# Kernel optimization log

Measured on AMD Instinct MI355X. Metric: run time of the kernel, lower is better.

Reference implementation:

```python
import jax, jax.numpy as jnp
import numpy as np

D = 256   # model dim
M = 64    # num mechanisms
B = 4
S = 8192


def setup_inputs() -> dict:
    key = jax.random.key(0)
    ks = jax.random.split(key, 16)
    n = jax.random.normal
    inp = {
        "x": n(ks[0], (B, S, D), jnp.float32),
        "context": n(ks[1], (B, S, D), jnp.float32),
        # stacked per-mechanism params (m, out, in) etc.
        "Wm": n(ks[2], (M, D, D), jnp.float32) * (1.0 / np.sqrt(D)),
        "bm": n(ks[3], (M, D), jnp.float32) * 0.02,
        "cm": n(ks[4], (M, D), jnp.float32),           # characteristics (1,1,dim) per node
        "um": n(ks[5], (M, D), jnp.float32) * (1.0 / np.sqrt(D)),  # timing_gate weight
        "vm": n(ks[6], (M,), jnp.float32) * 0.02,       # timing_gate bias
        # selector: Linear(d, 2d) -> GELU -> Linear(2d, m)
        "W1": n(ks[7], (2 * D, D), jnp.float32) * (1.0 / np.sqrt(D)),
        "b1": n(ks[8], (2 * D,), jnp.float32) * 0.02,
        "W2": n(ks[9], (M, 2 * D), jnp.float32) * (1.0 / np.sqrt(2 * D)),
        "b2": n(ks[10], (M,), jnp.float32) * 0.02,
        # integrate: Linear(2d, d)
        "Wi": n(ks[11], (D, 2 * D), jnp.float32) * (1.0 / np.sqrt(2 * D)),
        "bi": n(ks[12], (D,), jnp.float32) * 0.02,
    }
    return inp


def reference(x, context, Wm, bm, cm, um, vm, W1, b1, W2, b2, Wi, bi):
    # selector: softmax over mechanisms (b, s, m)
    h = jax.nn.gelu(jnp.einsum('bsd,ed->bse', context, W1) + b1, approximate=False)
    scores = jax.nn.softmax(jnp.einsum('bse,me->bsm', h, W2) + b2, axis=-1)

    # per-mechanism sigmoid timing gate (b, s, m)
    gate = jax.nn.sigmoid(jnp.einsum('bsd,md->bsm', x, um) + vm)

    # combined weight a[b,s,m] = softmax_score * gate; then
    # selected = sum_m a * (x @ Wm.T + bm + cm)  -- contracted without
    # materializing the (b, s, m, d) stack the torch loop builds.
    a = scores * gate                               # (b, s, m)
    selected = jnp.einsum('bsm,bse,mde->bsd', a, x, Wm) \
             + jnp.einsum('bsm,md->bsd', a, bm + cm)

    # integrate(concat([x, selected]))
    cat = jnp.concatenate([x, selected], axis=-1)   # (b, s, 2d)
    integrated = jnp.einsum('bse,de->bsd', cat, Wi) + bi
    return integrated
```

## Files before the change

### kernel.cpp

```cpp
#include <hip/hip_runtime.h>
#include <cstdint>
#include <cstddef>


typedef _Float16 f16;
typedef f16 f16x8 __attribute__((ext_vector_type(8)));
typedef float f32x4 __attribute__((ext_vector_type(4)));
typedef float f32x16 __attribute__((ext_vector_type(16)));

#define DEV __device__ __forceinline__

DEV uint32_t swz128(uint32_t b) { return b ^ (((b >> 7) & 7u) << 4); }

DEV void gload_lds16(const void* g, void* l) {
  __builtin_amdgcn_global_load_lds(
      (const __attribute__((address_space(1))) unsigned int*)g,
      (__attribute__((address_space(3))) unsigned int*)l, 16, 0, 0);
}

DEV f16x8 cvt8(float4 u0, float4 u1) {
  f16x8 v = {(f16)u0.x, (f16)u0.y, (f16)u0.z, (f16)u0.w,
             (f16)u1.x, (f16)u1.y, (f16)u1.z, (f16)u1.w};
  return v;
}

__global__ void prep_b_kernel(const float* __restrict__ S, f16* __restrict__ dst,
                              int K, int BN, int total) {
  int t = blockIdx.x * 256 + threadIdx.x;
  if (t >= total) return;
  int gpc = BN * 8;
  int g = t % gpc;
  int c = (t / gpc) % (K / 64);
  int cb = t / (gpc * (K / 64));
  int ks = g / (BN * 4);
  int rem = g % (BN * 4);
  int col = rem >> 2;
  int kg = rem & 3;
  int J = cb * BN + col;
  int k = c * 64 + ks * 32 + kg * 8;
  const float* s = S + (size_t)J * K + k;
  float4 u0 = *(const float4*)s;
  float4 u1 = *(const float4*)(s + 4);
  f16* chunk = dst + (size_t)(cb * (K / 64) + c) * (BN * 64);
  *(f16x8*)((char*)chunk + swz128((uint32_t)g * 16)) = cvt8(u0, u1);
}

__global__ void prep_wcat_kernel(const float* __restrict__ Wm,
                                 const float* __restrict__ bm,
                                 const float* __restrict__ cm,
                                 f16* __restrict__ dst) {
  int t = blockIdx.x * 256 + threadIdx.x;
  if (t >= 4 * 257 * 512) return;
  int g = t & 511;
  int gc = t >> 9;
  int c = gc % 257;
  int cb = gc / 257;
  int kstep = g >> 7;
  int khalf = (g >> 6) & 1;
  int col = cb * 64 + (g & 63);
  int k0 = kstep * 16 + khalf * 8;
  f16x8 v;
  if (c < 256) {
    int m = c & 63;
    int e0 = (c >> 6) * 64 + k0;
    const float* s = Wm + ((size_t)m * 256 + col) * 256 + e0;
    float4 u0 = *(const float4*)s;
    float4 u1 = *(const float4*)(s + 4);
    v = cvt8(u0, u1);
  } else {
#pragma unroll
    for (int j = 0; j < 8; ++j) {
      int k = k0 + j;
      v[j] = (f16)(bm[k * 256 + col] + cm[k * 256 + col]);
    }
  }
  *(f16x8*)(dst + ((size_t)(cb * 260 + c)) * 4096 + (size_t)g * 8) = v;
}

template <int BN, int NCHUNK, int A0C, int EPI>
__global__ __launch_bounds__(BN == 256 ? 512 : 256, 2)
void gemm_tpl(const float* __restrict__ A0, int lda0,
              const f16* __restrict__ A1, int lda1,
              const f16* __restrict__ Bt,
              const float* __restrict__ bias,
              float* __restrict__ outF, f16* __restrict__ outH, int ldo) {
  constexpr int WAVES = (BN == 256) ? 8 : 4;
  constexpr int THREADS = WAVES * 64;
  constexpr int WC = (BN == 256) ? 4 : 1;
  constexpr int WR = WAVES / WC;
  constexpr int RT = 128 / (WR * 16);
  constexpr int CT = (BN / WC) / 16;

  __shared__ alignas(16) f16 sA[2][128 * 64];
  __shared__ alignas(16) f16 sB[2][BN * 64];

  const int tid = threadIdx.x;
  const int lane = tid & 63;
  const int wid = tid >> 6;
  const int wr = wid / WC, wc = wid % WC;
  const int rb = blockIdx.x, cb = blockIdx.y;

  auto stageB = [&](int c, int buf) {
    const char* src = (const char*)(Bt + (size_t)(cb * NCHUNK + c) * (BN * 64));
#pragma unroll
    for (int it = 0; it < (BN * 64 * 2) / (THREADS * 16); ++it) {
      int off = (it * THREADS + tid) * 16;
      gload_lds16(src + off, (char*)&sB[buf][0] + off);
    }
  };
  auto stageA = [&](int c, int buf) {
#pragma unroll
    for (int it = 0; it < 1024 / THREADS; ++it) {
      int gg = it * THREADS + tid;
      int row = gg >> 3, eg = gg & 7;
      size_t rowG = (size_t)rb * 128 + row;
      f16x8 v;
      if (A0C > 0 && c < A0C) {
        const float* s = A0 + rowG * lda0 + c * 64 + eg * 8;
        float4 u0 = *(const float4*)s;
        float4 u1 = *(const float4*)(s + 4);
        v = cvt8(u0, u1);
      } else {
        v = *(const f16x8*)(A1 + rowG * lda1 + (c - A0C) * 64 + eg * 8);
      }
      *(f16x8*)((char*)&sA[buf][0] + swz128((uint32_t)(row * 128 + eg * 16))) = v;
    }
  };

  f32x4 acc[RT][CT];
#pragma unroll
  for (int i = 0; i < RT; ++i)
#pragma unroll
    for (int j = 0; j < CT; ++j) acc[i][j] = (f32x4){0.f, 0.f, 0.f, 0.f};

  stageB(0, 0);
  stageA(0, 0);
  __syncthreads();

  for (int c = 0; c < NCHUNK; ++c) {
    int cur = c & 1;
    if (c + 1 < NCHUNK) {
      stageB(c + 1, cur ^ 1);
      stageA(c + 1, cur ^ 1);
    }
#pragma unroll
    for (int ks = 0; ks < 2; ++ks) {
      f16x8 af[RT], bf[CT];
#pragma unroll
      for (int rt = 0; rt < RT; ++rt) {
        int row = wr * (RT * 16) + rt * 16 + (lane & 15);
        af[rt] = *(const f16x8*)((const char*)&sA[cur][0] +
                                 swz128((uint32_t)(row * 128 + ks * 64 + (lane >> 4) * 16)));
      }
#pragma unroll
      for (int ct = 0; ct < CT; ++ct) {
        int col = wc * (CT * 16) + ct * 16 + (lane & 15);
        bf[ct] = *(const f16x8*)((const char*)&sB[cur][0] +
                                 swz128((uint32_t)(((ks * BN + col) * 4 + (lane >> 4)) * 16)));
      }
#pragma unroll
      for (int rt = 0; rt < RT; ++rt)
#pragma unroll
        for (int ct = 0; ct < CT; ++ct)
          acc[rt][ct] = __builtin_amdgcn_mfma_f32_16x16x32_f16(af[rt], bf[ct], acc[rt][ct], 0, 0, 0);
    }
    __syncthreads();
  }

#pragma unroll
  for (int rt = 0; rt < RT; ++rt)
#pragma unroll
    for (int ct = 0; ct < CT; ++ct)
#pragma unroll
      for (int i = 0; i < 4; ++i) {
        size_t row = (size_t)rb * 128 + wr * (RT * 16) + rt * 16 + (lane >> 4) * 4 + i;
        int colG = cb * BN + wc * (CT * 16) + ct * 16 + (lane & 15);
        float v = acc[rt][ct][i];
        if constexpr (EPI == 0) {
          if (bias) v += bias[colG];
          outF[row * ldo + colG] = v;
        } else {
          v += bias[colG];
          float ge = 0.5f * v * (1.0f + erff(v * 0.70710678118f));
          outH[row * ldo + colG] = (f16)ge;
        }
      }
}

__global__ void selector_finish(const float* __restrict__ logits,
                                const float* __restrict__ glog,
                                const float* __restrict__ b2,
                                const float* __restrict__ vm,
                                f16* __restrict__ a16s) {
  int n = blockIdx.x * 4 + (threadIdx.x >> 6);
  int m = threadIdx.x & 63;
  float l = logits[(size_t)n * 64 + m] + b2[m];
  float mx = l;
#pragma unroll
  for (int o = 32; o; o >>= 1) mx = fmaxf(mx, __shfl_xor(mx, o));
  float p = expf(l - mx);
  float s = p;
#pragma unroll
  for (int o = 32; o; o >>= 1) s += __shfl_xor(s, o);
  float g = glog[(size_t)n * 64 + m] + vm[m];
  float gate = 1.0f / (1.0f + expf(-g));
  int rb6 = n >> 7, row = n & 127, gg = m >> 3, j = m & 7;
  a16s[(size_t)rb6 * 8192 + gg * 1024 + row * 8 + j] = (f16)(p / s * gate);
}

__global__ __launch_bounds__(128, 2)
void big_gemm(const float* __restrict__ x, const f16* __restrict__ a16s,
              const f16* __restrict__ Wcat, f16* __restrict__ sel) {
  __shared__ alignas(16) f16 sB[3][64 * 64];
  __shared__ alignas(16) f16 sAa[8 * 128 * 8];

  const int tid = threadIdx.x;
  const int lane = tid & 63;
  const int wid = tid >> 6;
  const int l31 = lane & 31;
  const int khalf = lane >> 5;
  const int bid = blockIdx.x;
  const int xcd = bid & 7;
  const int cb = xcd >> 1;
  const int rb = (xcd & 1) * 128 + (bid >> 3);
  const f16* Wb = Wcat + (size_t)cb * 260 * 4096;
  const int rbase = wid * 64 + l31;

  auto stageTo = [&](int c, char* dst) {
    const char* src = (const char*)(Wb + (size_t)c * 4096);
#pragma unroll
    for (int it = 0; it < 4; ++it) {
      int off = (it * 128 + tid) * 16;
      gload_lds16(src + off, dst + off);
    }
  };

  {
    const char* aSrc = (const char*)(a16s + (size_t)rb * 8192);
#pragma unroll
    for (int it = 0; it < 8; ++it) {
      int off = (it * 128 + tid) * 16;
      gload_lds16(aSrc + off, (char*)sAa + off);
    }
  }
  char* p0 = (char*)&sB[0][0];
  char* p1 = (char*)&sB[1][0];
  char* p2 = (char*)&sB[2][0];
  stageTo(0, p0);
  stageTo(1, p1);
  asm volatile("s_waitcnt vmcnt(4)" ::: "memory");
  __builtin_amdgcn_s_barrier();
  __builtin_amdgcn_sched_barrier(0);

  f32x16 acc[2][2];
#pragma unroll
  for (int i = 0; i < 2; ++i)
#pragma unroll
    for (int j = 0; j < 2; ++j)
#pragma unroll
      for (int r = 0; r < 16; ++r) acc[i][j][r] = 0.f;

  f16x8 xv[2][4];
  auto loadXV = [&](int er) {
#pragma unroll
    for (int rt = 0; rt < 2; ++rt)
#pragma unroll
      for (int ks = 0; ks < 4; ++ks) {
        const float* s = x + ((size_t)rb * 128 + rbase + rt * 32) * 256
                           + er * 64 + ks * 16 + khalf * 8;
        float4 u0 = *(const float4*)s;
        float4 u1 = *(const float4*)(s + 4);
        xv[rt][ks] = cvt8(u0, u1);
      }
  };

  f16x8 as_cur[2], as_nxt[2];
#pragma unroll
  for (int rt = 0; rt < 2; ++rt)
    as_cur[rt] = *(const f16x8*)((const char*)sAa + (rbase + rt * 32) * 16);

  const int bOff = khalf * 1024 + l31 * 16;
  f16x8 bf[2][8];
#pragma unroll
  for (int ks = 0; ks < 4; ++ks)
#pragma unroll
    for (int ct = 0; ct < 2; ++ct)
      bf[0][ks * 2 + ct] = *(const f16x8*)(p0 + bOff + ks * 2048 + ct * 512);

  for (int q8 = 0; q8 < 256; q8 += 8) {
    int gn = ((q8 + 8) & 63) >> 3;
#pragma unroll
    for (int rt = 0; rt < 2; ++rt)
      as_nxt[rt] = *(const f16x8*)((const char*)sAa + (gn * 128 + rbase + rt * 32) * 16);
    if ((q8 & 63) == 0) loadXV(q8 >> 6);
#pragma unroll
    for (int u = 0; u < 8; ++u) {
      const int q = q8 + u;
      stageTo(q + 2, p2);
      f16x8 af[2][4];
#pragma unroll
      for (int rt = 0; rt < 2; ++rt)
#pragma unroll
        for (int ks = 0; ks < 4; ++ks)
          af[rt][ks] = xv[rt][ks] * as_cur[rt][u];
      asm volatile("s_waitcnt vmcnt(4)" ::: "memory");
      __builtin_amdgcn_s_barrier();
      __builtin_amdgcn_sched_barrier(0);
      const char* nb = p1 + bOff;
#pragma unroll
      for (int ks = 0; ks < 4; ++ks)
#pragma unroll
        for (int ct = 0; ct < 2; ++ct)
          bf[(u + 1) & 1][ks * 2 + ct] = *(const f16x8*)(nb + ks * 2048 + ct * 512);
      __builtin_amdgcn_s_setprio(1);
#pragma unroll
      for (int ks = 0; ks < 4; ++ks)
#pragma unroll
        for (int rt = 0; rt < 2; ++rt)
#pragma unroll
          for (int ct = 0; ct < 2; ++ct)
            acc[rt][ct] = __builtin_amdgcn_mfma_f32_32x32x16_f16(
                af[rt][ks], bf[u & 1][ks * 2 + ct], acc[rt][ct], 0, 0, 0);
      __builtin_amdgcn_s_setprio(0);
      char* t = p0; p0 = p1; p1 = p2; p2 = t;
    }
    as_cur[0] = as_nxt[0];
    as_cur[1] = as_nxt[1];
  }

#pragma unroll
  for (int ks = 0; ks < 4; ++ks)
#pragma unroll
    for (int rt = 0; rt < 2; ++rt) {
      int g = ks * 2 + khalf;
      f16x8 af = *(const f16x8*)((const char*)sAa + (g * 128 + rbase + rt * 32) * 16);
#pragma unroll
      for (int ct = 0; ct < 2; ++ct)
        acc[rt][ct] = __builtin_amdgcn_mfma_f32_32x32x16_f16(
            af, bf[0][ks * 2 + ct], acc[rt][ct], 0, 0, 0);
    }

#pragma unroll
  for (int rt = 0; rt < 2; ++rt)
#pragma unroll
    for (int ct = 0; ct < 2; ++ct)
#pragma unroll
      for (int r = 0; r < 16; ++r) {
        int rowin = (r & 3) + 8 * (r >> 2) + 4 * khalf;
        size_t row = (size_t)rb * 128 + wid * 64 + rt * 32 + rowin;
        int col = cb * 64 + ct * 32 + l31;
        sel[row * 256 + col] = (f16)acc[rt][ct][r];
      }
}

extern "C" void kernel_launch(void* const* d_in, const int* in_sizes, int n_in,
                              void* d_out, int out_size, void* d_ws, size_t ws_size,
                              hipStream_t stream) {
  (void)in_sizes; (void)n_in; (void)out_size;
  const float* x   = (const float*)d_in[0];
  const float* ctx = (const float*)d_in[1];
  const float* Wm  = (const float*)d_in[2];
  const float* bm  = (const float*)d_in[3];
  const float* cm  = (const float*)d_in[4];
  const float* um  = (const float*)d_in[5];
  const float* vm  = (const float*)d_in[6];
  const float* W1  = (const float*)d_in[7];
  const float* b1  = (const float*)d_in[8];
  const float* W2  = (const float*)d_in[9];
  const float* b2  = (const float*)d_in[10];
  const float* Wi  = (const float*)d_in[11];
  const float* bi  = (const float*)d_in[12];
  float* out = (float*)d_out;

  char* ws = (char*)d_ws;
  size_t off = 0;
  f16* Wcat = (f16*)(ws + off); off += (size_t)4 * 260 * 4096 * 2;
  f16* W1t  = (f16*)(ws + off); off += (size_t)512 * 256 * 2;
  f16* W2t  = (f16*)(ws + off); off += (size_t)64 * 512 * 2;
  f16* umt  = (f16*)(ws + off); off += (size_t)64 * 256 * 2;
  f16* Wit  = (f16*)(ws + off); off += (size_t)256 * 512 * 2;
  f16* h16  = (f16*)(ws + off); off += (size_t)32768 * 512 * 2;
  float* logits = (float*)(ws + off); off += (size_t)32768 * 64 * 4;
  float* glog   = (float*)(ws + off); off += (size_t)32768 * 64 * 4;
  f16* a16s  = (f16*)(ws + off); off += (size_t)32768 * 64 * 2;
  f16* sel16 = (f16*)(ws + off); off += (size_t)32768 * 256 * 2;
  if (ws_size < off) return;

  prep_wcat_kernel<<<dim3(2056), dim3(256), 0, stream>>>(Wm, bm, cm, Wcat);
  prep_b_kernel<<<dim3(16384 / 256), dim3(256), 0, stream>>>(W1, W1t, 256, 256, 16384);
  prep_b_kernel<<<dim3(4096 / 256),  dim3(256), 0, stream>>>(W2, W2t, 512, 64, 4096);
  prep_b_kernel<<<dim3(2048 / 256),  dim3(256), 0, stream>>>(um, umt, 256, 64, 2048);
  prep_b_kernel<<<dim3(16384 / 256), dim3(256), 0, stream>>>(Wi, Wit, 512, 256, 16384);

  gemm_tpl<256, 4, 4, 1><<<dim3(256, 2), dim3(512), 0, stream>>>(
      ctx, 256, nullptr, 0, W1t, b1, nullptr, h16, 512);
  gemm_tpl<64, 4, 4, 0><<<dim3(256, 1), dim3(256), 0, stream>>>(
      x, 256, nullptr, 0, umt, nullptr, glog, nullptr, 64);
  gemm_tpl<64, 8, 0, 0><<<dim3(256, 1), dim3(256), 0, stream>>>(
      nullptr, 0, h16, 512, W2t, nullptr, logits, nullptr, 64);
  selector_finish<<<dim3(32768 / 4), dim3(256), 0, stream>>>(logits, glog, b2, vm, a16s);

  big_gemm<<<dim3(1024), dim3(128), 0, stream>>>(x, a16s, Wcat, sel16);

  gemm_tpl<256, 8, 4, 0><<<dim3(256, 1), dim3(512), 0, stream>>>(
      x, 256, sel16, 256, Wit, bi, out, nullptr, 256);
}
```

Baseline: 360.6 us.

## Double big_gemm row tile to 256 with 4 waves and paired weight staging

The big mixture GEMM now uses 256-thread blocks covering 256 rows, so each staged weight chunk is shared by four waves instead of two and half as many blocks are launched. Weight chunks are staged in pairs of 16 KB into a three-slot ring, with one barrier per pair instead of per chunk. The a16s layout in selector_finish is changed to match the 256-row tiling. This cuts global weight traffic and barrier count, at the cost of more LDS per block, fewer blocks in flight, and losing the register double-buffering of B fragments.

```diff
diff --git a/kernel.cpp b/kernel.cpp
--- a/kernel.cpp
+++ b/kernel.cpp
@@ -204,15 +204,15 @@
   for (int o = 32; o; o >>= 1) s += __shfl_xor(s, o);
   float g = glog[(size_t)n * 64 + m] + vm[m];
   float gate = 1.0f / (1.0f + expf(-g));
-  int rb6 = n >> 7, row = n & 127, gg = m >> 3, j = m & 7;
-  a16s[(size_t)rb6 * 8192 + gg * 1024 + row * 8 + j] = (f16)(p / s * gate);
-}
-
-__global__ __launch_bounds__(128, 2)
+  int rb = n >> 8, row = n & 255, gg = m >> 3, j = m & 7;
+  a16s[(size_t)rb * 16384 + gg * 2048 + row * 8 + j] = (f16)(p / s * gate);
+}
+
+__global__ __launch_bounds__(256, 2)
 void big_gemm(const float* __restrict__ x, const f16* __restrict__ a16s,
               const f16* __restrict__ Wcat, f16* __restrict__ sel) {
-  __shared__ alignas(16) f16 sB[3][64 * 64];
-  __shared__ alignas(16) f16 sAa[8 * 128 * 8];
+  __shared__ alignas(16) f16 sB[3][128 * 64];
+  __shared__ alignas(16) f16 sAa[8 * 256 * 8];
 
   const int tid = threadIdx.x;
   const int lane = tid & 63;
@@ -222,32 +222,32 @@
   const int bid = blockIdx.x;
   const int xcd = bid & 7;
   const int cb = xcd >> 1;
-  const int rb = (xcd & 1) * 128 + (bid >> 3);
+  const int rb = (xcd & 1) * 64 + (bid >> 3);
   const f16* Wb = Wcat + (size_t)cb * 260 * 4096;
   const int rbase = wid * 64 + l31;
 
-  auto stageTo = [&](int c, char* dst) {
-    const char* src = (const char*)(Wb + (size_t)c * 4096);
+  char* const sBbase = (char*)&sB[0][0];
+
+  auto stagePair = [&](int p, int slotIdx) {
+    const char* src = (const char*)Wb + (size_t)p * 16384;
+    char* dst = sBbase + slotIdx * 16384;
 #pragma unroll
     for (int it = 0; it < 4; ++it) {
-      int off = (it * 128 + tid) * 16;
+      int off = (it * 256 + tid) * 16;
       gload_lds16(src + off, dst + off);
     }
   };
 
   {
-    const char* aSrc = (const char*)(a16s + (size_t)rb * 8192);
+    const char* aSrc = (const char*)(a16s + (size_t)rb * 16384);
 #pragma unroll
     for (int it = 0; it < 8; ++it) {
-      int off = (it * 128 + tid) * 16;
+      int off = (it * 256 + tid) * 16;
       gload_lds16(aSrc + off, (char*)sAa + off);
     }
   }
-  char* p0 = (char*)&sB[0][0];
-  char* p1 = (char*)&sB[1][0];
-  char* p2 = (char*)&sB[2][0];
-  stageTo(0, p0);
-  stageTo(1, p1);
+  stagePair(0, 0);
+  stagePair(1, 1);
   asm volatile("s_waitcnt vmcnt(4)" ::: "memory");
   __builtin_amdgcn_s_barrier();
   __builtin_amdgcn_sched_barrier(0);
@@ -266,7 +266,7 @@
     for (int rt = 0; rt < 2; ++rt)
 #pragma unroll
       for (int ks = 0; ks < 4; ++ks) {
-        const float* s = x + ((size_t)rb * 128 + rbase + rt * 32) * 256
+        const float* s = x + ((size_t)rb * 256 + rbase + rt * 32) * 256
                            + er * 64 + ks * 16 + khalf * 8;
         float4 u0 = *(const float4*)s;
         float4 u1 = *(const float4*)(s + 4);
@@ -274,44 +274,40 @@
       }
   };
 
-  f16x8 as_cur[2], as_nxt[2];
-#pragma unroll
-  for (int rt = 0; rt < 2; ++rt)
-    as_cur[rt] = *(const f16x8*)((const char*)sAa + (rbase + rt * 32) * 16);
-
   const int bOff = khalf * 1024 + l31 * 16;
-  f16x8 bf[2][8];
-#pragma unroll
-  for (int ks = 0; ks < 4; ++ks)
-#pragma unroll
-    for (int ct = 0; ct < 2; ++ct)
-      bf[0][ks * 2 + ct] = *(const f16x8*)(p0 + bOff + ks * 2048 + ct * 512);
-
-  for (int q8 = 0; q8 < 256; q8 += 8) {
-    int gn = ((q8 + 8) & 63) >> 3;
-#pragma unroll
-    for (int rt = 0; rt < 2; ++rt)
-      as_nxt[rt] = *(const f16x8*)((const char*)sAa + (gn * 128 + rbase + rt * 32) * 16);
+
+  for (int q8g = 0; q8g < 32; ++q8g) {
+    const int q8 = q8g * 8;
     if ((q8 & 63) == 0) loadXV(q8 >> 6);
-#pragma unroll
-    for (int u = 0; u < 8; ++u) {
-      const int q = q8 + u;
-      stageTo(q + 2, p2);
-      f16x8 af[2][4];
+    f16x8 as_cur[2];
+    {
+      int g = (q8 & 63) >> 3;
 #pragma unroll
       for (int rt = 0; rt < 2; ++rt)
+        as_cur[rt] = *(const f16x8*)((const char*)sAa + ((g * 256) + rbase + rt * 32) * 16);
+    }
+#pragma unroll
+    for (int p = 0; p < 4; ++p) {
+      const int pj = (q8 >> 1) + p;
+      f16x8 af0[2][4];
+#pragma unroll
+      for (int rt = 0; rt < 2; ++rt)
 #pragma unroll
         for (int ks = 0; ks < 4; ++ks)
-          af[rt][ks] = xv[rt][ks] * as_cur[rt][u];
+          af0[rt][ks] = xv[rt][ks] * as_cur[rt][2 * p + 0];
       asm volatile("s_waitcnt vmcnt(4)" ::: "memory");
       __builtin_amdgcn_s_barrier();
       __builtin_amdgcn_sched_barrier(0);
-      const char* nb = p1 + bOff;
+      stagePair(pj + 2, (pj + 2) % 3);
+      const char* base = sBbase + (pj % 3) * 16384 + bOff;
+      f16x8 bfA[8], bfB[8];
 #pragma unroll
       for (int ks = 0; ks < 4; ++ks)
 #pragma unroll
-        for (int ct = 0; ct < 2; ++ct)
-          bf[(u + 1) & 1][ks * 2 + ct] = *(const f16x8*)(nb + ks * 2048 + ct * 512);
+        for (int ct = 0; ct < 2; ++ct) {
+          bfA[ks * 2 + ct] = *(const f16x8*)(base + ks * 2048 + ct * 512);
+          bfB[ks * 2 + ct] = *(const f16x8*)(base + 8192 + ks * 2048 + ct * 512);
+        }
       __builtin_amdgcn_s_setprio(1);
 #pragma unroll
       for (int ks = 0; ks < 4; ++ks)
@@ -320,24 +316,40 @@
 #pragma unroll
           for (int ct = 0; ct < 2; ++ct)
             acc[rt][ct] = __builtin_amdgcn_mfma_f32_32x32x16_f16(
-                af[rt][ks], bf[u & 1][ks * 2 + ct], acc[rt][ct], 0, 0, 0);
+                af0[rt][ks], bfA[ks * 2 + ct], acc[rt][ct], 0, 0, 0);
       __builtin_amdgcn_s_setprio(0);
-      char* t = p0; p0 = p1; p1 = p2; p2 = t;
-    }
-    as_cur[0] = as_nxt[0];
-    as_cur[1] = as_nxt[1];
+      f16x8 af1[2][4];
+#pragma unroll
+      for (int rt = 0; rt < 2; ++rt)
+#pragma unroll
+        for (int ks = 0; ks < 4; ++ks)
+          af1[rt][ks] = xv[rt][ks] * as_cur[rt][2 * p + 1];
+      __builtin_amdgcn_s_setprio(1);
+#pragma unroll
+      for (int ks = 0; ks < 4; ++ks)
+#pragma unroll
+        for (int rt = 0; rt < 2; ++rt)
+#pragma unroll
+          for (int ct = 0; ct < 2; ++ct)
+            acc[rt][ct] = __builtin_amdgcn_mfma_f32_32x32x16_f16(
+                af1[rt][ks], bfB[ks * 2 + ct], acc[rt][ct], 0, 0, 0);
+      __builtin_amdgcn_s_setprio(0);
+    }
   }
 
+  asm volatile("s_waitcnt vmcnt(4)" ::: "memory");
+  __builtin_amdgcn_s_barrier();
 #pragma unroll
   for (int ks = 0; ks < 4; ++ks)
 #pragma unroll
     for (int rt = 0; rt < 2; ++rt) {
       int g = ks * 2 + khalf;
-      f16x8 af = *(const f16x8*)((const char*)sAa + (g * 128 + rbase + rt * 32) * 16);
-#pragma unroll
-      for (int ct = 0; ct < 2; ++ct)
-        acc[rt][ct] = __builtin_amdgcn_mfma_f32_32x32x16_f16(
-            af, bf[0][ks * 2 + ct], acc[rt][ct], 0, 0, 0);
+      f16x8 af = *(const f16x8*)((const char*)sAa + ((g * 256) + rbase + rt * 32) * 16);
+#pragma unroll
+      for (int ct = 0; ct < 2; ++ct) {
+        f16x8 bf = *(const f16x8*)(sBbase + 2 * 16384 + bOff + ks * 2048 + ct * 512);
+        acc[rt][ct] = __builtin_amdgcn_mfma_f32_32x32x16_f16(af, bf, acc[rt][ct], 0, 0, 0);
+      }
     }
 
 #pragma unroll
@@ -347,7 +359,7 @@
 #pragma unroll
       for (int r = 0; r < 16; ++r) {
         int rowin = (r & 3) + 8 * (r >> 2) + 4 * khalf;
-        size_t row = (size_t)rb * 128 + wid * 64 + rt * 32 + rowin;
+        size_t row = (size_t)rb * 256 + wid * 64 + rt * 32 + rowin;
         int col = cb * 64 + ct * 32 + l31;
         sel[row * 256 + col] = (f16)acc[rt][ct][r];
       }
@@ -400,7 +412,7 @@
       nullptr, 0, h16, 512, W2t, nullptr, logits, nullptr, 64);
   selector_finish<<<dim3(32768 / 4), dim3(256), 0, stream>>>(logits, glog, b2, vm, a16s);
 
-  big_gemm<<<dim3(1024), dim3(128), 0, stream>>>(x, a16s, Wcat, sel16);
+  big_gemm<<<dim3(512), dim3(256), 0, stream>>>(x, a16s, Wcat, sel16);
 
   gemm_tpl<256, 8, 4, 0><<<dim3(256, 1), dim3(512), 0, stream>>>(
       x, 256, sel16, 256, Wit, bi, out, nullptr, 256);
```

Result: faster. 351.0 us (-2.7%).
